# Kernel optimization log

Measured on AMD Instinct MI355X. Metric: run time of the kernel, lower is better.

The kernel has to match this reference:

```python
import jax, jax.numpy as jnp
import numpy as np
from jax import lax

B, S, V = 16, 512, 32000
EMB, LM = 256, 768
H, L = 512, 2            # lstm_hidden_size, num_layers
D_IN = LM + EMB          # 1024, equals 2*H so both layers share weight shapes
HID, C = 1024, 5


def _lstm_dir(xs, mask, Wi, Wh, bi, bh, reverse):
    """One direction of one LSTM layer, packed-sequence semantics.
    xs: [B,S,D], mask: [B,S,1] float (1 where t < length).
    Gate order matches torch: i, f, g, o."""
    xg = jnp.einsum('bsd,gd->bsg', xs, Wi) + bi + bh  # [B,S,4H]
    if reverse:
        xg = xg[:, ::-1]
        m = mask[:, ::-1]
    else:
        m = mask
    b = xs.shape[0]
    h0 = jnp.zeros((b, H), xs.dtype)
    c0 = jnp.zeros((b, H), xs.dtype)

    def step(carry, inp):
        h, c = carry
        xg_t, m_t = inp  # [B,4H], [B,1]
        g = xg_t + h @ Wh.T
        i, f, gg, o = jnp.split(g, 4, axis=-1)
        i = jax.nn.sigmoid(i); f = jax.nn.sigmoid(f)
        gg = jnp.tanh(gg); o = jax.nn.sigmoid(o)
        c_new = f * c + i * gg
        h_new = o * jnp.tanh(c_new)
        # packed-sequence: state only advances on valid steps, outputs zero on pads
        h2 = jnp.where(m_t > 0, h_new, h)
        c2 = jnp.where(m_t > 0, c_new, c)
        return (h2, c2), h_new * m_t

    _, ys = lax.scan(step, (h0, c0), (xg.transpose(1, 0, 2), m.transpose(1, 0, 2)))
    ys = ys.transpose(1, 0, 2)  # [B,S,H]
    if reverse:
        ys = ys[:, ::-1]
    return ys


def setup_inputs() -> dict:
    key = jax.random.key(0)
    ks = jax.random.split(key, 16)
    sc = 1.0 / np.sqrt(H)
    x = jax.random.randint(ks[0], (B, S), 0, V, dtype=jnp.int32)
    lengths = jax.random.randint(ks[1], (B,), 1, S + 1, dtype=jnp.int32)
    lang_emb = jax.random.normal(ks[2], (B, S, LM), jnp.float32)
    emb_table = (jax.random.normal(ks[3], (V, EMB), jnp.float32) * 0.02).at[0].set(0.0)  # padding_idx=0
    W_ih = jax.random.uniform(ks[4], (L, 2, 4 * H, D_IN), jnp.float32, -sc, sc)
    W_hh = jax.random.uniform(ks[5], (L, 2, 4 * H, H), jnp.float32, -sc, sc)
    b_ih = jax.random.uniform(ks[6], (L, 2, 4 * H), jnp.float32, -sc, sc)
    b_hh = jax.random.uniform(ks[7], (L, 2, 4 * H), jnp.float32, -sc, sc)
    W1 = jax.random.normal(ks[8], (HID, 2 * H), jnp.float32) * 0.02
    b1 = jnp.zeros((HID,), jnp.float32)
    W2 = jax.random.normal(ks[9], (HID, HID), jnp.float32) * 0.02
    b2 = jnp.zeros((HID,), jnp.float32)
    W3 = jax.random.normal(ks[10], (C, HID), jnp.float32) * 0.02
    b3 = jnp.zeros((C,), jnp.float32)
    return {"x": x, "lengths": lengths, "lang_emb": lang_emb, "emb_table": emb_table,
            "W_ih": W_ih, "W_hh": W_hh, "b_ih": b_ih, "b_hh": b_hh,
            "W1": W1, "b1": b1, "W2": W2, "b2": b2, "W3": W3, "b3": b3}


def reference(x, lengths, lang_emb, emb_table, W_ih, W_hh, b_ih, b_hh,
              W1, b1, W2, b2, W3, b3):
    mask = (jnp.arange(S)[None, :] < lengths[:, None]).astype(lang_emb.dtype)[..., None]  # [B,S,1]
    h = jnp.concatenate([lang_emb, emb_table[x]], axis=2)  # [B,S,1024]
    for l in range(L):
        fwd = _lstm_dir(h, mask, W_ih[l, 0], W_hh[l, 0], b_ih[l, 0], b_hh[l, 0], False)
        bwd = _lstm_dir(h, mask, W_ih[l, 1], W_hh[l, 1], b_ih[l, 1], b_hh[l, 1], True)
        h = jnp.concatenate([fwd, bwd], axis=-1)  # [B,S,2H]; inter-layer dropout is eval-mode identity
    # vectorized MLP head (the torch loop over timesteps, fused over B*S); dropout = identity (eval)
    a1 = jax.nn.leaky_relu(jnp.einsum('bsd,hd->bsh', h, W1) + b1)
    a2 = jax.nn.leaky_relu(jnp.einsum('bsh,gh->bsg', a1, W2) + b2)
    out = jnp.einsum('bsg,cg->bsc', a2, W3) + b3  # [B,S,C]
    return out
```

## Files before the change

kernel.cpp:

```cpp
#include <hip/hip_runtime.h>


typedef unsigned short u16;
typedef unsigned int   u32;
typedef unsigned long long u64;
typedef short s16x8 __attribute__((ext_vector_type(8)));
typedef float f32x4 __attribute__((ext_vector_type(4)));

#define SENT32 0x7F7F7F7Fu

__device__ __forceinline__ float b2f(u16 h) { return __uint_as_float(((u32)h) << 16); }
__device__ __forceinline__ u16 f2b(float x) {
  u32 u = __float_as_uint(x);
  return (u16)((u + 0x7fffu + ((u >> 16) & 1u)) >> 16);
}
__device__ __forceinline__ void packA3(float v0, float v1, u32& w0, u32& w1, u32& w2) {
  u16 h0 = f2b(v0), h1 = f2b(v1);
  u16 l0 = f2b(v0 - b2f(h0)), l1 = f2b(v1 - b2f(h1));
  w0 = (u32)h0 | ((u32)l0 << 16);
  w1 = (u32)h0 | ((u32)h1 << 16);
  w2 = (u32)l1 | ((u32)h1 << 16);
}
__device__ __forceinline__ void packB3(float v0, float v1, u32& w0, u32& w1, u32& w2) {
  u16 h0 = f2b(v0), h1 = f2b(v1);
  u16 l0 = f2b(v0 - b2f(h0)), l1 = f2b(v1 - b2f(h1));
  w0 = (u32)h0 | ((u32)h0 << 16);
  w1 = (u32)l0 | ((u32)h1 << 16);
  w2 = (u32)h1 | ((u32)l1 << 16);
}

__global__ __launch_bounds__(256) void k_embed(const int* __restrict__ x,
    const float* __restrict__ lang, const float* __restrict__ emb, u16* __restrict__ A3) {
  const int m = blockIdx.x;
  const int k = threadIdx.x * 4;
  const float* src = (k < 768) ? (lang + (size_t)m * 768 + k)
                               : (emb + (size_t)x[m] * 256 + (k - 768));
  float4 v = *(const float4*)src;
  u32 w0, w1, w2, w3, w4, w5;
  packA3(v.x, v.y, w0, w1, w2);
  packA3(v.z, v.w, w3, w4, w5);
  uint2* dst = (uint2*)(A3 + (size_t)m * 3072 + 3 * k);
  dst[0] = make_uint2(w0, w1); dst[1] = make_uint2(w2, w3); dst[2] = make_uint2(w4, w5);
}

__global__ __launch_bounds__(256) void k_prepw(const float* __restrict__ W,
    u16* __restrict__ W3, int nq) {
  const int idx = blockIdx.x * 256 + threadIdx.x;
  if (idx >= nq) return;
  const int base = idx * 4, row = base >> 10, k = base & 1023;
  float4 v = *(const float4*)(W + base);
  u32 w0, w1, w2, w3, w4, w5;
  packB3(v.x, v.y, w0, w1, w2);
  packB3(v.z, v.w, w3, w4, w5);
  uint2* dst = (uint2*)(W3 + (size_t)row * 3072 + 3 * k);
  dst[0] = make_uint2(w0, w1); dst[1] = make_uint2(w2, w3); dst[2] = make_uint2(w4, w5);
}
__global__ __launch_bounds__(256) void k_prepwh(const float* __restrict__ W,
    u16* __restrict__ hi) {
  const int idx = blockIdx.x * 256 + threadIdx.x;
  const int base = idx * 4;
  float4 v = *(const float4*)(W + base);
  float vv[4] = {v.x, v.y, v.z, v.w};
  u16 h[4];
#pragma unroll
  for (int i = 0; i < 4; ++i) h[i] = f2b(vv[i]);
  *(uint2*)(hi + base) = make_uint2((u32)h[0] | ((u32)h[1] << 16), (u32)h[2] | ((u32)h[3] << 16));
}
__global__ __launch_bounds__(256) void k_prepb(const float* __restrict__ bih,
    const float* __restrict__ bhh, float* __restrict__ bsum) {
  const int tid = blockIdx.x * 256 + threadIdx.x;
  bsum[tid] = bih[tid] + bhh[tid];
}
__global__ __launch_bounds__(256) void k_tri(const float* __restrict__ act, u16* __restrict__ A3) {
  const int idx = blockIdx.x * 256 + threadIdx.x;
  const int base = idx * 4, row = base >> 10, k = base & 1023;
  float4 v = *(const float4*)(act + base);
  u32 w0, w1, w2, w3, w4, w5;
  packA3(v.x, v.y, w0, w1, w2);
  packA3(v.z, v.w, w3, w4, w5);
  uint2* dst = (uint2*)(A3 + (size_t)row * 3072 + 3 * k);
  dst[0] = make_uint2(w0, w1); dst[1] = make_uint2(w2, w3); dst[2] = make_uint2(w4, w5);
}

template <int EPI>
__global__ __launch_bounds__(256) void k_gemm(const u16* __restrict__ A,
    const u16* __restrict__ B, const float* __restrict__ bias, float* __restrict__ outp,
    int Ka, int N) {
  __shared__ u16 As[4096];
  __shared__ u16 Bs[4096];
  const int tid = threadIdx.x, wave = tid >> 6, lane = tid & 63;
  const int bm0 = blockIdx.x * 128, bn0 = blockIdx.y * 128;
  const int wm = (wave & 1) * 64, wn = (wave >> 1) * 64;
  const int kq = (lane >> 4) * 8;
  f32x4 acc[4][4];
#pragma unroll
  for (int i = 0; i < 4; ++i)
#pragma unroll
    for (int j = 0; j < 4; ++j) acc[i][j] = (f32x4){0.f, 0.f, 0.f, 0.f};

  const int srow = tid >> 2, soff = (tid & 3) * 8;
  const u16* Ag  = A + (size_t)(bm0 + srow) * Ka + soff;
  const u16* Ag2 = Ag + (size_t)64 * Ka;
  const u16* Bg  = B + (size_t)(bn0 + srow) * Ka + soff;
  const u16* Bg2 = Bg + (size_t)64 * Ka;
  u16* sA = As + wave * 512;
  u16* sB = Bs + wave * 512;

  for (int k0 = 0; k0 < Ka; k0 += 32) {
    __syncthreads();
    __builtin_amdgcn_global_load_lds((const __attribute__((address_space(1))) void*)(Ag + k0),
        (__attribute__((address_space(3))) void*)sA, 16, 0, 0);
    __builtin_amdgcn_global_load_lds((const __attribute__((address_space(1))) void*)(Ag2 + k0),
        (__attribute__((address_space(3))) void*)(sA + 2048), 16, 0, 0);
    __builtin_amdgcn_global_load_lds((const __attribute__((address_space(1))) void*)(Bg + k0),
        (__attribute__((address_space(3))) void*)sB, 16, 0, 0);
    __builtin_amdgcn_global_load_lds((const __attribute__((address_space(1))) void*)(Bg2 + k0),
        (__attribute__((address_space(3))) void*)(sB + 2048), 16, 0, 0);
    __syncthreads();
    s16x8 af[4], bf[4];
#pragma unroll
    for (int mi = 0; mi < 4; ++mi) af[mi] = *(const s16x8*)(As + (wm + mi * 16 + (lane & 15)) * 32 + kq);
#pragma unroll
    for (int ni = 0; ni < 4; ++ni) bf[ni] = *(const s16x8*)(Bs + (wn + ni * 16 + (lane & 15)) * 32 + kq);
#pragma unroll
    for (int mi = 0; mi < 4; ++mi)
#pragma unroll
      for (int ni = 0; ni < 4; ++ni)
        acc[mi][ni] = __builtin_amdgcn_mfma_f32_16x16x32_bf16(af[mi], bf[ni], acc[mi][ni], 0, 0, 0);
  }

#pragma unroll
  for (int mi = 0; mi < 4; ++mi)
#pragma unroll
    for (int r = 0; r < 4; ++r) {
      const int m = bm0 + wm + mi * 16 + (lane >> 4) * 4 + r;
#pragma unroll
      for (int ni = 0; ni < 4; ++ni) {
        const int n = bn0 + wn + ni * 16 + (lane & 15);
        float v = acc[mi][ni][r] + bias[n];
        if (EPI == 0) {
          const size_t off = (size_t)(n >> 11) * 16777216u
                           + (size_t)((m & 511) * 16 + (m >> 9)) * 2048 + (n & 2047);
          outp[off] = v;
        } else {
          v = (v > 0.f) ? v : 0.01f * v;
          outp[(size_t)m * N + n] = v;
        }
      }
    }
}

__global__ __launch_bounds__(256, 1) void k_rec(const float* __restrict__ xg,
    const u16* __restrict__ WhiP, const int* __restrict__ lens, u16* __restrict__ Yt,
    u16* __restrict__ stepA, u16* __restrict__ stepB) {
  __shared__ u16 hs[2 * 16 * 520];
  __shared__ float gx[4][16][33];
  const int tid = threadIdx.x, wave = tid >> 6, lane = tid & 63;
  const int dir = blockIdx.x >> 4, slice = blockIdx.x & 15, ubase = slice * 32;
  const int kq = (lane >> 4) * 8;
  const int col = lane & 15;
  const int bq = (lane >> 4) * 4;

  s16x8 bfrag[2][16];
#pragma unroll
  for (int j = 0; j < 2; ++j) {
    const u16* wr = WhiP + ((size_t)dir * 2048 + wave * 512 + ubase + j * 16 + col) * 512 + kq;
#pragma unroll
    for (int kt = 0; kt < 16; ++kt) bfrag[j][kt] = *(const s16x8*)(wr + kt * 32);
  }
  const int pp = tid & 15, bb = tid >> 4;
  const int len_b = lens[bb];
  float c0 = 0.f, h0v = 0.f, c1 = 0.f, h1v = 0.f;
  const float* xgp = xg + (size_t)dir * 16777216u;
  const int sp = tid >> 7, srow = (tid & 127) >> 3, soff = tid & 7;

  for (int s = 0; s < 512; ++s) {
    const int t = dir ? (511 - s) : s;
    const float* xr = xgp + ((size_t)t * 16 + bq) * 2048 + wave * 512 + ubase + col;
    f32x4 a0, a1;
    a0[0] = xr[0];  a0[1] = xr[2048]; a0[2] = xr[4096]; a0[3] = xr[6144];
    a1[0] = xr[16]; a1[1] = xr[2064]; a1[2] = xr[4112]; a1[3] = xr[6160];

    if (s > 0) {
      const int g = dir * 512 + s;
      const u64* slot64 = (const u64*)((g < 768) ? (stepA + (size_t)g * 16384)
                                                 : (stepB + (size_t)(g - 768) * 16384));
      const u64* src = slot64 + sp * 2048 + srow * 128 + soff;
      u64 wv[16];
      bool ok;
      do {
#pragma unroll
        for (int i = 0; i < 16; ++i)
          wv[i] = __hip_atomic_load(src + i * 8, __ATOMIC_RELAXED, __HIP_MEMORY_SCOPE_AGENT);
        ok = true;
#pragma unroll
        for (int i = 0; i < 16; ++i)
          ok &= ((u32)wv[i] != SENT32) & ((u32)(wv[i] >> 32) != SENT32);
      } while (!ok);
      u64* drow = (u64*)(hs + sp * 8320 + srow * 520);
#pragma unroll
      for (int i = 0; i < 16; ++i) drow[soff + i * 8] = wv[i];
    }
    __syncthreads();
    if (s > 0) {
      f32x4 l0 = (f32x4){0.f, 0.f, 0.f, 0.f}, l1 = (f32x4){0.f, 0.f, 0.f, 0.f};
      const u16* hh = hs + col * 520 + kq;
      const u16* hl = hh + 8320;
#pragma unroll
      for (int kt = 0; kt < 16; ++kt) {
        s16x8 ah = *(const s16x8*)(hh + kt * 32);
        s16x8 al = *(const s16x8*)(hl + kt * 32);
        a0 = __builtin_amdgcn_mfma_f32_16x16x32_bf16(ah, bfrag[0][kt], a0, 0, 0, 0);
        a1 = __builtin_amdgcn_mfma_f32_16x16x32_bf16(ah, bfrag[1][kt], a1, 0, 0, 0);
        l0 = __builtin_amdgcn_mfma_f32_16x16x32_bf16(al, bfrag[0][kt], l0, 0, 0, 0);
        l1 = __builtin_amdgcn_mfma_f32_16x16x32_bf16(al, bfrag[1][kt], l1, 0, 0, 0);
      }
      a0 += l0; a1 += l1;
    }
#pragma unroll
    for (int r = 0; r < 4; ++r) {
      gx[wave][bq + r][col] = a0[r];
      gx[wave][bq + r][16 + col] = a1[r];
    }
    __syncthreads();

    const int u0 = 2 * pp, u1 = u0 + 1;
    const float gi0 = gx[0][bb][u0], gf0 = gx[1][bb][u0], gg0 = gx[2][bb][u0], go0 = gx[3][bb][u0];
    const float gi1 = gx[0][bb][u1], gf1 = gx[1][bb][u1], gg1 = gx[2][bb][u1], go1 = gx[3][bb][u1];
    const float ii0 = 1.f / (1.f + __expf(-gi0)),  ii1 = 1.f / (1.f + __expf(-gi1));
    const float ff0 = 1.f / (1.f + __expf(-gf0)),  ff1 = 1.f / (1.f + __expf(-gf1));
    const float gz0 = 1.f - 2.f / (__expf(2.f * gg0) + 1.f);
    const float gz1 = 1.f - 2.f / (__expf(2.f * gg1) + 1.f);
    const float oo0 = 1.f / (1.f + __expf(-go0)),  oo1 = 1.f / (1.f + __expf(-go1));
    const float cn0 = ff0 * c0 + ii0 * gz0,        cn1 = ff1 * c1 + ii1 * gz1;
    const float hn0 = oo0 * (1.f - 2.f / (__expf(2.f * cn0) + 1.f));
    const float hn1 = oo1 * (1.f - 2.f / (__expf(2.f * cn1) + 1.f));
    const bool mk = (t < len_b);
    c0 = mk ? cn0 : c0;  h0v = mk ? hn0 : h0v;
    c1 = mk ? cn1 : c1;  h1v = mk ? hn1 : h1v;
    const float y0 = mk ? hn0 : 0.f, y1 = mk ? hn1 : 0.f;

    if (s < 511) {
      const u16 s0h = f2b(h0v), s0l = f2b(h0v - b2f(s0h));
      const u16 s1h = f2b(h1v), s1l = f2b(h1v - b2f(s1h));
      const int gw = dir * 512 + s + 1;
      u16* slot = (gw < 768) ? (stepA + (size_t)gw * 16384)
                             : (stepB + (size_t)(gw - 768) * 16384);
      u32* dh = (u32*)(slot + (size_t)bb * 512 + ubase) + pp;
      u32* dl = (u32*)(slot + 8192 + (size_t)bb * 512 + ubase) + pp;
      __hip_atomic_store(dh, (u32)s0h | ((u32)s1h << 16), __ATOMIC_RELAXED, __HIP_MEMORY_SCOPE_AGENT);
      __hip_atomic_store(dl, (u32)s0l | ((u32)s1l << 16), __ATOMIC_RELAXED, __HIP_MEMORY_SCOPE_AGENT);
    }

    u32 w0, w1, w2;
    packA3(y0, y1, w0, w1, w2);
    const int ug = dir * 512 + ubase + u0;
    u32* yp = (u32*)(Yt + (size_t)(bb * 512 + t) * 3072 + 3 * ug);
    yp[0] = w0; yp[1] = w1; yp[2] = w2;
  }
}

__global__ __launch_bounds__(256) void k_head(const float* __restrict__ a2,
    const float* __restrict__ W3, const float* __restrict__ b3, float* __restrict__ out) {
  const int m = (blockIdx.x * 256 + threadIdx.x) >> 6;
  const int lane = threadIdx.x & 63;
  const float* row = a2 + (size_t)m * 1024;
  float s[5] = {0.f, 0.f, 0.f, 0.f, 0.f};
  for (int j = lane; j < 1024; j += 64) {
    const float v = row[j];
#pragma unroll
    for (int c = 0; c < 5; ++c) s[c] += v * W3[c * 1024 + j];
  }
#pragma unroll
  for (int c = 0; c < 5; ++c)
    for (int off = 32; off > 0; off >>= 1) s[c] += __shfl_down(s[c], off, 64);
  if (lane == 0)
#pragma unroll
    for (int c = 0; c < 5; ++c) out[(size_t)m * 5 + c] = s[c] + b3[c];
}

extern "C" void kernel_launch(void* const* d_in, const int* in_sizes, int n_in,
                              void* d_out, int out_size, void* d_ws, size_t ws_size,
                              hipStream_t stream) {
  const int*   x    = (const int*)d_in[0];
  const int*   lens = (const int*)d_in[1];
  const float* lang = (const float*)d_in[2];
  const float* emb  = (const float*)d_in[3];
  const float* Wih  = (const float*)d_in[4];
  const float* Whh  = (const float*)d_in[5];
  const float* bih  = (const float*)d_in[6];
  const float* bhh  = (const float*)d_in[7];
  const float* W1   = (const float*)d_in[8];
  const float* b1   = (const float*)d_in[9];
  const float* W2   = (const float*)d_in[10];
  const float* b2   = (const float*)d_in[11];
  const float* W3   = (const float*)d_in[12];
  const float* b3   = (const float*)d_in[13];
  float* out = (float*)d_out;
  char* ws = (char*)d_ws;

  float* xg     = (float*)(ws + 0);
  float* act    = (float*)(ws + 0);
  u16*   A3     = (u16*)(ws + 134217728);
  u16*   wb3    = (u16*)(ws + 184549376);
  u16*   stepA  = (u16*)(ws + 184549376);
  u16*   whh_hi = (u16*)(ws + 209715200);
  u16*   stepB  = (u16*)(ws + 218103808);
  u16*   w3b    = (u16*)(ws + 226492416);
  float* bsum   = (float*)(ws + 233046016);

  k_prepb<<<32, 256, 0, stream>>>(bih, bhh, bsum);
  k_prepwh<<<4096, 256, 0, stream>>>(Whh, whh_hi);
  k_embed<<<8192, 256, 0, stream>>>(x, lang, emb, A3);

  k_prepw<<<4096, 256, 0, stream>>>(Wih, wb3, 1048576);
  k_gemm<0><<<dim3(64, 32), 256, 0, stream>>>(A3, wb3, bsum, xg, 3072, 4096);
  hipMemsetAsync(stepA, 0x7F, 25165824, stream);
  hipMemsetAsync(stepB, 0x7F, 8388608, stream);
  k_rec<<<32, 256, 0, stream>>>(xg, whh_hi, lens, A3, stepA, stepB);
  k_prepw<<<4096, 256, 0, stream>>>(Wih + 4194304, wb3, 1048576);
  k_gemm<0><<<dim3(64, 32), 256, 0, stream>>>(A3, wb3, bsum + 4096, xg, 3072, 4096);
  hipMemsetAsync(stepA, 0x7F, 25165824, stream);
  hipMemsetAsync(stepB, 0x7F, 8388608, stream);
  k_rec<<<32, 256, 0, stream>>>(xg, whh_hi + 2097152, lens, A3, stepA, stepB);
  k_prepw<<<1024, 256, 0, stream>>>(W1, w3b, 262144);
  k_gemm<1><<<dim3(64, 8), 256, 0, stream>>>(A3, w3b, b1, act, 3072, 1024);
  k_tri<<<8192, 256, 0, stream>>>(act, A3);
  k_prepw<<<1024, 256, 0, stream>>>(W2, w3b, 262144);
  k_gemm<1><<<dim3(64, 8), 256, 0, stream>>>(A3, w3b, b2, act, 3072, 1024);
  k_head<<<2048, 256, 0, stream>>>(act, W3, b3, out);
}
```

Measured before the change: 3.846 ms.

## Load recurrent h state directly into MFMA fragment registers, dropping LDS staging

The step buffer now uses a fragment-major layout for h, so each wave polls and loads its MFMA A-operands straight from global memory into registers. This removes the shared-memory h staging and one __syncthreads per timestep. The gate scratch buffer is double-buffered to avoid a write-after-read hazard without a second barrier. The trade-off is that every wave redundantly reads the full h slice from L2, and the spin loop gains s_sleep backoff and an iteration guard.

Measured after the change: 5.482 ms. 42.5% more time.

```diff
diff --git a/kernel.cpp b/kernel.cpp
--- a/kernel.cpp
+++ b/kernel.cpp
@@ -153,8 +153,7 @@
 __global__ __launch_bounds__(256, 1) void k_rec(const float* __restrict__ xg,
     const u16* __restrict__ WhiP, const int* __restrict__ lens, u16* __restrict__ Yt,
     u16* __restrict__ stepA, u16* __restrict__ stepB) {
-  __shared__ u16 hs[2 * 16 * 520];
-  __shared__ float gx[4][16][33];
+  __shared__ float gx[2][4][16][33];
   const int tid = threadIdx.x, wave = tid >> 6, lane = tid & 63;
   const int dir = blockIdx.x >> 4, slice = blockIdx.x & 15, ubase = slice * 32;
   const int kq = (lane >> 4) * 8;
@@ -172,7 +171,7 @@
   const int len_b = lens[bb];
   float c0 = 0.f, h0v = 0.f, c1 = 0.f, h1v = 0.f;
   const float* xgp = xg + (size_t)dir * 16777216u;
-  const int sp = tid >> 7, srow = (tid & 127) >> 3, soff = tid & 7;
+  const int pu = slice * 512 + ((((2 * pp) >> 3) * 16) + bb) * 8 + ((2 * pp) & 7);
 
   for (int s = 0; s < 512; ++s) {
     const int t = dir ? (511 - s) : s;
@@ -183,56 +182,68 @@
 
     if (s > 0) {
       const int g = dir * 512 + s;
-      const u64* slot64 = (const u64*)((g < 768) ? (stepA + (size_t)g * 16384)
-                                                 : (stepB + (size_t)(g - 768) * 16384));
-      const u64* src = slot64 + sp * 2048 + srow * 128 + soff;
-      u64 wv[16];
-      bool ok;
+      const u16* slot = (g < 768) ? (stepA + (size_t)g * 16384)
+                                  : (stepB + (size_t)(g - 768) * 16384);
+      const u64* ph = (const u64*)slot + lane * 2;
+      const u64* pl = ph + 2048;
+      u64 dh[32], dl[32];
+      bool ok; int guard;
+      guard = 0;
       do {
 #pragma unroll
-        for (int i = 0; i < 16; ++i)
-          wv[i] = __hip_atomic_load(src + i * 8, __ATOMIC_RELAXED, __HIP_MEMORY_SCOPE_AGENT);
+        for (int kt = 0; kt < 16; ++kt) {
+          dh[2 * kt]     = __hip_atomic_load(ph + kt * 128,     __ATOMIC_RELAXED, __HIP_MEMORY_SCOPE_AGENT);
+          dh[2 * kt + 1] = __hip_atomic_load(ph + kt * 128 + 1, __ATOMIC_RELAXED, __HIP_MEMORY_SCOPE_AGENT);
+        }
         ok = true;
 #pragma unroll
-        for (int i = 0; i < 16; ++i)
-          ok &= ((u32)wv[i] != SENT32) & ((u32)(wv[i] >> 32) != SENT32);
-      } while (!ok);
-      u64* drow = (u64*)(hs + sp * 8320 + srow * 520);
-#pragma unroll
-      for (int i = 0; i < 16; ++i) drow[soff + i * 8] = wv[i];
-    }
-    __syncthreads();
-    if (s > 0) {
+        for (int i = 0; i < 32; ++i)
+          ok &= ((u32)dh[i] != SENT32) & ((u32)(dh[i] >> 32) != SENT32);
+        if (!ok) __builtin_amdgcn_s_sleep(1);
+      } while (!ok && ++guard < (1 << 17));
+      guard = 0;
+      do {
+#pragma unroll
+        for (int kt = 0; kt < 16; ++kt) {
+          dl[2 * kt]     = __hip_atomic_load(pl + kt * 128,     __ATOMIC_RELAXED, __HIP_MEMORY_SCOPE_AGENT);
+          dl[2 * kt + 1] = __hip_atomic_load(pl + kt * 128 + 1, __ATOMIC_RELAXED, __HIP_MEMORY_SCOPE_AGENT);
+        }
+        ok = true;
+#pragma unroll
+        for (int i = 0; i < 32; ++i)
+          ok &= ((u32)dl[i] != SENT32) & ((u32)(dl[i] >> 32) != SENT32);
+        if (!ok) __builtin_amdgcn_s_sleep(1);
+      } while (!ok && ++guard < (1 << 17));
       f32x4 l0 = (f32x4){0.f, 0.f, 0.f, 0.f}, l1 = (f32x4){0.f, 0.f, 0.f, 0.f};
-      const u16* hh = hs + col * 520 + kq;
-      const u16* hl = hh + 8320;
 #pragma unroll
       for (int kt = 0; kt < 16; ++kt) {
-        s16x8 ah = *(const s16x8*)(hh + kt * 32);
-        s16x8 al = *(const s16x8*)(hl + kt * 32);
-        a0 = __builtin_amdgcn_mfma_f32_16x16x32_bf16(ah, bfrag[0][kt], a0, 0, 0, 0);
-        a1 = __builtin_amdgcn_mfma_f32_16x16x32_bf16(ah, bfrag[1][kt], a1, 0, 0, 0);
-        l0 = __builtin_amdgcn_mfma_f32_16x16x32_bf16(al, bfrag[0][kt], l0, 0, 0, 0);
-        l1 = __builtin_amdgcn_mfma_f32_16x16x32_bf16(al, bfrag[1][kt], l1, 0, 0, 0);
+        union { u64 q[2]; s16x8 v; } ah, al;
+        ah.q[0] = dh[2 * kt]; ah.q[1] = dh[2 * kt + 1];
+        al.q[0] = dl[2 * kt]; al.q[1] = dl[2 * kt + 1];
+        a0 = __builtin_amdgcn_mfma_f32_16x16x32_bf16(ah.v, bfrag[0][kt], a0, 0, 0, 0);
+        a1 = __builtin_amdgcn_mfma_f32_16x16x32_bf16(ah.v, bfrag[1][kt], a1, 0, 0, 0);
+        l0 = __builtin_amdgcn_mfma_f32_16x16x32_bf16(al.v, bfrag[0][kt], l0, 0, 0, 0);
+        l1 = __builtin_amdgcn_mfma_f32_16x16x32_bf16(al.v, bfrag[1][kt], l1, 0, 0, 0);
       }
       a0 += l0; a1 += l1;
     }
+    float (*gz)[16][33] = gx[s & 1];
 #pragma unroll
     for (int r = 0; r < 4; ++r) {
-      gx[wave][bq + r][col] = a0[r];
-      gx[wave][bq + r][16 + col] = a1[r];
+      gz[wave][bq + r][col] = a0[r];
+      gz[wave][bq + r][16 + col] = a1[r];
     }
     __syncthreads();
 
     const int u0 = 2 * pp, u1 = u0 + 1;
-    const float gi0 = gx[0][bb][u0], gf0 = gx[1][bb][u0], gg0 = gx[2][bb][u0], go0 = gx[3][bb][u0];
-    const float gi1 = gx[0][bb][u1], gf1 = gx[1][bb][u1], gg1 = gx[2][bb][u1], go1 = gx[3][bb][u1];
+    const float gi0 = gz[0][bb][u0], gf0 = gz[1][bb][u0], gg0 = gz[2][bb][u0], go0 = gz[3][bb][u0];
+    const float gi1 = gz[0][bb][u1], gf1 = gz[1][bb][u1], gg1 = gz[2][bb][u1], go1 = gz[3][bb][u1];
     const float ii0 = 1.f / (1.f + __expf(-gi0)),  ii1 = 1.f / (1.f + __expf(-gi1));
     const float ff0 = 1.f / (1.f + __expf(-gf0)),  ff1 = 1.f / (1.f + __expf(-gf1));
-    const float gz0 = 1.f - 2.f / (__expf(2.f * gg0) + 1.f);
-    const float gz1 = 1.f - 2.f / (__expf(2.f * gg1) + 1.f);
+    const float gt0 = 1.f - 2.f / (__expf(2.f * gg0) + 1.f);
+    const float gt1 = 1.f - 2.f / (__expf(2.f * gg1) + 1.f);
     const float oo0 = 1.f / (1.f + __expf(-go0)),  oo1 = 1.f / (1.f + __expf(-go1));
-    const float cn0 = ff0 * c0 + ii0 * gz0,        cn1 = ff1 * c1 + ii1 * gz1;
+    const float cn0 = ff0 * c0 + ii0 * gt0,        cn1 = ff1 * c1 + ii1 * gt1;
     const float hn0 = oo0 * (1.f - 2.f / (__expf(2.f * cn0) + 1.f));
     const float hn1 = oo1 * (1.f - 2.f / (__expf(2.f * cn1) + 1.f));
     const bool mk = (t < len_b);
@@ -244,13 +255,14 @@
       const u16 s0h = f2b(h0v), s0l = f2b(h0v - b2f(s0h));
       const u16 s1h = f2b(h1v), s1l = f2b(h1v - b2f(s1h));
       const int gw = dir * 512 + s + 1;
-      u16* slot = (gw < 768) ? (stepA + (size_t)gw * 16384)
-                             : (stepB + (size_t)(gw - 768) * 16384);
-      u32* dh = (u32*)(slot + (size_t)bb * 512 + ubase) + pp;
-      u32* dl = (u32*)(slot + 8192 + (size_t)bb * 512 + ubase) + pp;
+      u16* slotW = (gw < 768) ? (stepA + (size_t)gw * 16384)
+                              : (stepB + (size_t)(gw - 768) * 16384);
+      u32* dh = (u32*)slotW + (pu >> 1);
+      u32* dl = (u32*)(slotW + 8192) + (pu >> 1);
       __hip_atomic_store(dh, (u32)s0h | ((u32)s1h << 16), __ATOMIC_RELAXED, __HIP_MEMORY_SCOPE_AGENT);
       __hip_atomic_store(dl, (u32)s0l | ((u32)s1l << 16), __ATOMIC_RELAXED, __HIP_MEMORY_SCOPE_AGENT);
     }
+    __builtin_amdgcn_sched_barrier(0);
 
     u32 w0, w1, w2;
     packA3(y0, y1, w0, w1, w2);
```
